# Optimization experiments

Hardware: AMD Instinct MI355X
Metric: run time of the kernel (lower is better)

Reference implementation:

```python
import jax, jax.numpy as jnp
import numpy as np
import math

B, S, D, H, DFF = 2, 2048, 1024, 16, 4096
DK = D // H
EPS = 1e-6


def setup_inputs() -> dict:
    key = jax.random.key(0)
    ks = jax.random.split(key, 12)
    s = 0.02
    return {
        "x": jax.random.normal(ks[0], (B, S, D), jnp.float32),
        "mask": jnp.ones((B, S), jnp.int32),
        "wq": jax.random.normal(ks[1], (D, D), jnp.float32) * s,
        "bq": jnp.zeros((D,), jnp.float32),
        "wk": jax.random.normal(ks[2], (D, D), jnp.float32) * s,
        "bk": jnp.zeros((D,), jnp.float32),
        "wv": jax.random.normal(ks[3], (D, D), jnp.float32) * s,
        "bv": jnp.zeros((D,), jnp.float32),
        "wo": jax.random.normal(ks[4], (D, D), jnp.float32) * s,
        "bo": jnp.zeros((D,), jnp.float32),
        "g1": jnp.ones((D,), jnp.float32),
        "b1": jnp.zeros((D,), jnp.float32),
        "g2": jnp.ones((D,), jnp.float32),
        "b2": jnp.zeros((D,), jnp.float32),
        "w1": jax.random.normal(ks[5], (DFF, D), jnp.float32) * s,
        "bf1": jnp.zeros((DFF,), jnp.float32),
        "w2": jax.random.normal(ks[6], (D, DFF), jnp.float32) * s,
        "bf2": jnp.zeros((D,), jnp.float32),
    }


def _gelu(x):
    # x * 0.5 * (1 + erf(x / sqrt(2))) -- exact erf-based GELU as in source
    return x * 0.5 * (1.0 + jax.lax.erf(x * (1.0 / math.sqrt(2.0))))


def _layernorm(x, gamma, beta):
    # torch.std uses unbiased (ddof=1); eps is OUTSIDE the sqrt in the source
    mean = jnp.mean(x, axis=-1, keepdims=True)
    std = jnp.std(x, axis=-1, keepdims=True, ddof=1)
    return gamma * (x - mean) / (std + EPS) + beta


def _block(x, mask, wq, bq, wk, bk, wv, bv, wo, bo, g1, b1, g2, b2, w1, bf1, w2, bf2):
    # multi-head attention (dropout is identity in eval mode)
    q = (x @ wq.T + bq).reshape(B, S, H, DK).transpose(0, 2, 1, 3)  # bhsd
    k = (x @ wk.T + bk).reshape(B, S, H, DK).transpose(0, 2, 1, 3)
    v = (x @ wv.T + bv).reshape(B, S, H, DK).transpose(0, 2, 1, 3)
    scores = jnp.einsum("bhsd,bhtd->bhst", q, k) / math.sqrt(DK)
    scores = jnp.where(mask[:, None, None, :] == 0, -1e9, scores)
    attn = jax.nn.softmax(scores, axis=-1)
    cv = jnp.einsum("bhst,bhtd->bhsd", attn, v)
    cv = cv.transpose(0, 2, 1, 3).reshape(B, S, D)
    hd = cv @ wo.T + bo
    # residual + norm1
    hd = _layernorm(x + hd, g1, b1)
    # position-wise FFN with erf GELU
    ff = _gelu(hd @ w1.T + bf1) @ w2.T + bf2
    return _layernorm(hd + ff, g2, b2)


def reference(x, mask, wq, bq, wk, bk, wv, bv, wo, bo, g1, b1, g2, b2, w1, bf1, w2, bf2):
    return _block(x, mask, wq, bq, wk, bk, wv, bv, wo, bo, g1, b1, g2, b2, w1, bf1, w2, bf2)
```

## Files before the change

### kernel.cpp

```cpp
#include <hip/hip_runtime.h>
#include <hip/hip_bf16.h>

#define B_   2
#define S_   2048
#define D_   1024
#define H_   16
#define DK_  64
#define DFF_ 4096
#define M_   (B_*S_)

typedef unsigned short u16;
typedef __attribute__((ext_vector_type(8))) short short8;
typedef __attribute__((ext_vector_type(4))) short bf16x4;
typedef __attribute__((ext_vector_type(4))) float floatx4;

__device__ __forceinline__ u16 f2bf(float f) {
    union { float f; unsigned u; } v; v.f = f;
    unsigned r = v.u + 0x7fffu + ((v.u >> 16) & 1u);
    return (u16)(r >> 16);
}
__device__ __forceinline__ u16 f2bf_fast(float f) {
    __hip_bfloat16 h = __float2bfloat16(f);
    return *reinterpret_cast<u16*>(&h);
}

__device__ __forceinline__ float exp2_fast(float f) {
    return __builtin_amdgcn_exp2f(f);
}

__device__ __forceinline__ void g2l16(const u16* g, u16* l) {
    __builtin_amdgcn_global_load_lds((const __attribute__((address_space(1))) void*)g,
                                     (__attribute__((address_space(3))) void*)l,
                                     16, 0, 0);
}

__device__ __forceinline__ unsigned lds_off(const void* p) {
    return (unsigned)(unsigned long long)p;
}

#define TRB16(dst, va, IMM)                                                    \
    asm volatile("ds_read_b64_tr_b16 %0, %1 offset:" #IMM                      \
                 : "=v"(dst) : "v"(va))

__global__ __launch_bounds__(256) void cvt_all(
    const float* __restrict__ x,  const float* __restrict__ wq,
    const float* __restrict__ wk, const float* __restrict__ wv,
    const float* __restrict__ wo, const float* __restrict__ w1,
    const float* __restrict__ w2,
    u16* __restrict__ xb, u16* __restrict__ wqkvb, u16* __restrict__ wob,
    u16* __restrict__ w1b, u16* __restrict__ w2b) {
    for (int i = blockIdx.x * 256 + threadIdx.x; i < 4194304;
         i += gridDim.x * 256) {
        const float* s; u16* d; int off;
        if (i < 1048576)      { s = x;  d = xb;    off = i; }
        else if (i < 1310720) { s = wq; d = wqkvb; off = i - 1048576; }
        else if (i < 1572864) { s = wk; d = wqkvb + 1048576; off = i - 1310720; }
        else if (i < 1835008) { s = wv; d = wqkvb + 2097152; off = i - 1572864; }
        else if (i < 2097152) { s = wo; d = wob;   off = i - 1835008; }
        else if (i < 3145728) { s = w1; d = w1b;   off = i - 2097152; }
        else                  { s = w2; d = w2b;   off = i - 3145728; }
        float4 v = reinterpret_cast<const float4*>(s)[off];
        ushort4 o;
        o.x = f2bf(v.x); o.y = f2bf(v.y); o.z = f2bf(v.z); o.w = f2bf(v.w);
        reinterpret_cast<ushort4*>(d)[off] = o;
    }
}

__global__ __launch_bounds__(256) void prep_misc(const float* __restrict__ bq,
                                                 const float* __restrict__ bk,
                                                 const float* __restrict__ bv,
                                                 const int* __restrict__ mask,
                                                 float* __restrict__ bqkv,
                                                 float* __restrict__ mbias) {
    int i = blockIdx.x * 256 + threadIdx.x;
    if (i < 3 * D_) {
        float v = (i < D_) ? bq[i] : (i < 2 * D_) ? bk[i - D_] : bv[i - 2 * D_];
        bqkv[i] = v;
    } else if (i < 3 * D_ + B_ * S_) {
        int k = i - 3 * D_;
        mbias[k] = (mask[k] == 0) ? -1.44269504e9f : 0.0f;
    }
}

template <int EPI>
__global__ __launch_bounds__(512, 2) void gemm256_bt(const u16* __restrict__ A,
                                                     const u16* __restrict__ Bw,
                                                     const float* __restrict__ bias,
                                                     u16* __restrict__ Cb,
                                                     int N, int K) {
    __shared__ alignas(16) u16 sA[2][2][8192];
    __shared__ alignas(16) u16 sB[2][2][8192];
    const int tid = threadIdx.x;
    const int wid = tid >> 6, lane = tid & 63;
    const int lrow = lane & 15, lgrp = lane >> 4;
    const int wm = wid >> 2, wn = wid & 3;

    const int nbx = gridDim.x;
    const int nwg = nbx * gridDim.y;
    const int orig = blockIdx.y * nbx + blockIdx.x;
    const int qd = nwg >> 3, rr = nwg & 7, xc = orig & 7, oi = orig >> 3;
    const int swz = (xc < rr ? xc * (qd + 1) : rr * (qd + 1) + (xc - rr) * qd) + oi;
    const int m0 = (swz % nbx) * 256, n0 = (swz / nbx) * 256;

    const u16* Ab = A + (size_t)m0 * K;
    const u16* Bb = Bw + (size_t)n0 * K;
    const int T = K >> 6;

    const int c0 = (wid * 2 + 0) * 64 + lane;
    const int c1 = (wid * 2 + 1) * 64 + lane;
    const int r0 = c0 >> 3, g0 = c0 & 7;
    const int r1 = c1 >> 3, g1 = c1 & 7;
    const size_t so0 = (size_t)r0 * K + (size_t)((g0 ^ (r0 & 7)) * 8);
    const size_t so1 = (size_t)r1 * K + (size_t)((g1 ^ (r1 & 7)) * 8);
    const int d0 = (wid * 2 + 0) * 512;
    const int d1 = (wid * 2 + 1) * 512;

    auto stageA = [&](int par, int half, int kt) {
        const u16* src = Ab + (size_t)(half * 128) * K + kt * 64;
        g2l16(src + so0, &sA[par][half][d0]);
        g2l16(src + so1, &sA[par][half][d1]);
    };
    auto stageB = [&](int par, int half, int kt) {
        const u16* src = Bb + (size_t)(half * 128) * K + kt * 64;
        g2l16(src + so0, &sB[par][half][d0]);
        g2l16(src + so1, &sB[par][half][d1]);
    };

    stageA(0, 0, 0); stageA(0, 1, 0);
    stageB(0, 0, 0); stageB(0, 1, 0);
    if (T > 1) { stageB(1, 0, 1); stageB(1, 1, 1); }
    asm volatile("s_waitcnt vmcnt(4)" ::: "memory");
    asm volatile("s_barrier" ::: "memory");

    floatx4 acc[8][4] = {};
    const int rbase = (wn & 1) * 64;
    const int bhalf = wn >> 1;

    for (int t = 0; t < T; t++) {
        const int par = t & 1;
        const char* baseA = (const char*)&sA[par][wm][0];
        const char* baseB = (const char*)&sB[par][bhalf][0];
        short8 bfr[4][2];
#pragma unroll
        for (int ph = 0; ph < 4; ph++) {
            if (ph == 0) {
#pragma unroll
                for (int nj = 0; nj < 4; nj++) {
                    int rb = rbase + nj * 16 + lrow;
#pragma unroll
                    for (int kk = 0; kk < 2; kk++) {
                        int off = rb * 128 + (((kk * 4 + lgrp) ^ (lrow & 7)) * 16);
                        bfr[nj][kk] = *reinterpret_cast<const short8*>(baseB + off);
                    }
                }
            }
            short8 af[2][2];
#pragma unroll
            for (int a = 0; a < 2; a++) {
                int ra = (2 * ph + a) * 16 + lrow;
#pragma unroll
                for (int kk = 0; kk < 2; kk++) {
                    int off = ra * 128 + (((kk * 4 + lgrp) ^ (lrow & 7)) * 16);
                    af[a][kk] = *reinterpret_cast<const short8*>(baseA + off);
                }
            }
            if (ph == 0) { if (t + 1 < T) stageA(par ^ 1, 0, t + 1); }
            if (ph == 1) { if (t + 1 < T) stageA(par ^ 1, 1, t + 1); }
            if (ph == 2) { if (t + 2 < T) stageB(par, 0, t + 2); }
            if (ph == 3) { if (t + 2 < T) stageB(par, 1, t + 2); }

            asm volatile("s_barrier" ::: "memory");
            asm volatile("s_waitcnt lgkmcnt(0)" ::: "memory");
            __builtin_amdgcn_sched_barrier(0);

            __builtin_amdgcn_s_setprio(1);
#pragma unroll
            for (int a = 0; a < 2; a++)
#pragma unroll
                for (int nj = 0; nj < 4; nj++) {
                    acc[2 * ph + a][nj] = __builtin_amdgcn_mfma_f32_16x16x32_bf16(
                        af[a][0], bfr[nj][0], acc[2 * ph + a][nj], 0, 0, 0);
                    acc[2 * ph + a][nj] = __builtin_amdgcn_mfma_f32_16x16x32_bf16(
                        af[a][1], bfr[nj][1], acc[2 * ph + a][nj], 0, 0, 0);
                }
            __builtin_amdgcn_s_setprio(0);

            if (ph == 3) {
                if (t >= T - 3) asm volatile("s_waitcnt vmcnt(0)" ::: "memory");
                else            asm volatile("s_waitcnt vmcnt(4)" ::: "memory");
            }
            asm volatile("s_barrier" ::: "memory");
        }
    }

#pragma unroll
    for (int mi = 0; mi < 8; mi++) {
        int row = m0 + wm * 128 + mi * 16 + lgrp * 4;
#pragma unroll
        for (int nj = 0; nj < 4; nj++) {
            int col = n0 + wn * 64 + nj * 16 + lrow;
            float bc = bias[col];
#pragma unroll
            for (int j = 0; j < 4; j++) {
                float v = acc[mi][nj][j] + bc;
                if (EPI == 2) v = 0.5f * v * (1.0f + erff(v * 0.70710678118654752f));
                Cb[(size_t)(row + j) * N + col] = f2bf(v);
            }
        }
    }
}

template <int SPLIT>
__global__ __launch_bounds__(256) void gemm_sk(const u16* __restrict__ A,
                                               const u16* __restrict__ Bw,
                                               const float* __restrict__ bias,
                                               float* __restrict__ Cf,
                                               int N, int K) {
    __shared__ u16 sA[128 * 32];
    __shared__ u16 sB[128 * 32];
    const int tid = threadIdx.x;
    const int wid = tid >> 6, lane = tid & 63;
    const int lrow = lane & 15, lgrp = lane >> 4;
    const int z = blockIdx.z;
    const int Kc = K / SPLIT;

    const int nbx = gridDim.x;
    const int nwg = nbx * gridDim.y;
    const int orig = blockIdx.y * nbx + blockIdx.x;
    const int qd = nwg >> 3, rr = nwg & 7, xc = orig & 7, oi = orig >> 3;
    const int swz = (xc < rr ? xc * (qd + 1) : rr * (qd + 1) + (xc - rr) * qd) + oi;
    const int m0 = (swz % nbx) * 128, n0 = (swz / nbx) * 128;

    const int wm = wid >> 1, wn = wid & 1;
    const int ar = lane >> 2, ac = lane & 3;

    floatx4 acc[4][4] = {};
    const u16* Ab = A + (size_t)m0 * K;
    const u16* Bb = Bw + (size_t)n0 * K;
    float* Co = Cf + (size_t)z * M_ * N;

    for (int k0 = z * Kc; k0 < (z + 1) * Kc; k0 += 32) {
#pragma unroll
        for (int i = 0; i < 2; i++) {
            int seg = wid * 2 + i;
            int row = seg * 16 + ar;
            g2l16(Ab + (size_t)row * K + k0 + ac * 8, &sA[seg * 512]);
            g2l16(Bb + (size_t)row * K + k0 + ac * 8, &sB[seg * 512]);
        }
        __syncthreads();
        short8 af[4], bfr[4];
#pragma unroll
        for (int mi = 0; mi < 4; mi++)
            af[mi] = *reinterpret_cast<const short8*>(
                &sA[(wm * 64 + mi * 16 + lrow) * 32 + lgrp * 8]);
#pragma unroll
        for (int ni = 0; ni < 4; ni++)
            bfr[ni] = *reinterpret_cast<const short8*>(
                &sB[(wn * 64 + ni * 16 + lrow) * 32 + lgrp * 8]);
#pragma unroll
        for (int mi = 0; mi < 4; mi++)
#pragma unroll
            for (int ni = 0; ni < 4; ni++)
                acc[mi][ni] = __builtin_amdgcn_mfma_f32_16x16x32_bf16(
                    af[mi], bfr[ni], acc[mi][ni], 0, 0, 0);
        __syncthreads();
    }

#pragma unroll
    for (int mi = 0; mi < 4; mi++) {
        int row = m0 + wm * 64 + mi * 16 + lgrp * 4;
#pragma unroll
        for (int ni = 0; ni < 4; ni++) {
            int col = n0 + wn * 64 + ni * 16 + lrow;
            float bc = (z == 0) ? bias[col] : 0.0f;
#pragma unroll
            for (int j = 0; j < 4; j++)
                Co[(size_t)(row + j) * N + col] = acc[mi][ni][j] + bc;
        }
    }
}

__global__ __launch_bounds__(512) void attn_kernel(const u16* __restrict__ QKV,
                                                   const float* __restrict__ mbias,
                                                   u16* __restrict__ O) {
    const int SD = 3 * D_;
    __shared__ alignas(16) u16 ktL[2][4096];
    __shared__ alignas(16) u16 vtL[2][4096];
    __shared__ alignas(16) u16 pL[8][1024];

    const int orig = blockIdx.y * gridDim.x + blockIdx.x;
    const int swz = (orig & 7) * 64 + (orig >> 3);
    const int qt = swz & 15, bh = swz >> 4;
    const int b = bh >> 4, h = bh & 15;

    const int tid = threadIdx.x, wid = tid >> 6, lane = tid & 63;
    const int lrow = lane & 15, lgrp = lane >> 4;

    const u16* Qp = QKV + h * DK_;
    const u16* Kp = QKV + D_ + h * DK_;
    const u16* Vp = QKV + 2 * D_ + h * DK_;
    const float* mbrow = mbias + b * S_;

    const int qr = qt * 128 + wid * 16 + lrow;
    const u16* qrow = Qp + (size_t)(b * S_ + qr) * SD;
    short8 aq0 = *reinterpret_cast<const short8*>(qrow + lgrp * 8);
    short8 aq1 = *reinterpret_cast<const short8*>(qrow + 32 + lgrp * 8);

    const int q8 = wid * 64 + lane;
    const int krow = q8 >> 3, kcb = q8 & 7;
    const u16* kq = Kp + (size_t)(b * S_ + krow) * SD + ((kcb ^ (krow & 7)) * 8);
    const int ov = wid * 512 + lane * 8;
    const int vk = ((ov >> 6) & 7) * 8 + ((ov >> 9) & 1) * 4 + ((ov >> 4) & 3);
    const int vd = (ov >> 10) * 16 + (ov & 8);
    const u16* vq = Vp + (size_t)(b * S_ + vk) * SD + vd;

    auto issue = [&](int bufIdx) {
        g2l16(kq, &ktL[bufIdx][wid * 512]);
        g2l16(vq, &vtL[bufIdx][wid * 512]);
        kq += 64 * SD;
        vq += 64 * SD;
    };

    floatx4 accO[4] = {};
    float mrun = -1e30f, lrun = 0.f;
    const float SC2 = 0.18033688011112042f;

    issue(0);
    int cur = 0;
    for (int t = 0; t < S_ / 64; t++) {
        const int kv0 = t * 64;
        if (t < S_ / 64 - 1) {
            issue(cur ^ 1);
            asm volatile("s_waitcnt vmcnt(2)" ::: "memory");
        } else {
            asm volatile("s_waitcnt vmcnt(0)" ::: "memory");
        }
        __builtin_amdgcn_s_barrier();
        asm volatile("" ::: "memory");

        const u16* ktc = ktL[cur];
        const unsigned vva = lds_off(vtL[cur]) + lane * 8;

        float4 mb[4];
#pragma unroll
        for (int ni = 0; ni < 4; ni++)
            mb[ni] = *reinterpret_cast<const float4*>(mbrow + kv0 + ni * 16 + lgrp * 4);

        floatx4 st[4];
        __builtin_amdgcn_s_setprio(1);
#pragma unroll
        for (int ni = 0; ni < 4; ni++) {
            int row = ni * 16 + lrow;
            int off0 = (row * 128 + lgrp * 16) ^ ((lrow & 7) << 4);
            int off1 = (row * 128 + 64 + lgrp * 16) ^ ((lrow & 7) << 4);
            short8 bk0 = *reinterpret_cast<const short8*>((const char*)ktc + off0);
            short8 bk1 = *reinterpret_cast<const short8*>((const char*)ktc + off1);
            floatx4 z = {0.f, 0.f, 0.f, 0.f};
            z = __builtin_amdgcn_mfma_f32_16x16x32_bf16(bk0, aq0, z, 0, 0, 0);
            z = __builtin_amdgcn_mfma_f32_16x16x32_bf16(bk1, aq1, z, 0, 0, 0);
            st[ni] = z;
        }
        __builtin_amdgcn_s_setprio(0);

        bf16x4 vt0[4], vt1[4], vt2[4], vt3[4];
#pragma unroll
        for (int nd = 0; nd < 4; nd++) {
            unsigned a = vva + nd * 2048;
            TRB16(vt0[nd], a, 0);
            TRB16(vt1[nd], a, 1024);
            TRB16(vt2[nd], a, 512);
            TRB16(vt3[nd], a, 1536);
        }

        float pm[4][4];
#pragma unroll
        for (int ni = 0; ni < 4; ni++) {
            const float* mbp = reinterpret_cast<const float*>(&mb[ni]);
#pragma unroll
            for (int j = 0; j < 4; j++)
                pm[ni][j] = fmaf(st[ni][j], SC2, mbp[j]);
        }
        float pmax = pm[0][0];
#pragma unroll
        for (int ni = 0; ni < 4; ni++)
#pragma unroll
            for (int j = 0; j < 4; j++) pmax = fmaxf(pmax, pm[ni][j]);
        pmax = fmaxf(pmax, __shfl_xor(pmax, 16, 64));
        pmax = fmaxf(pmax, __shfl_xor(pmax, 32, 64));

        bool upd = !__all(pmax - mrun <= 11.5f);
        float fac = 1.0f;
        if (upd) {
            float mn = fmaxf(mrun, pmax);
            fac = exp2_fast(mrun - mn);
            mrun = mn;
        }

        float p[4][4];
        float s = 0.f;
#pragma unroll
        for (int ni = 0; ni < 4; ni++)
#pragma unroll
            for (int j = 0; j < 4; j++) {
                float e = exp2_fast(pm[ni][j] - mrun);
                p[ni][j] = e;
                s += e;
            }
        s += __shfl_xor(s, 16, 64);
        s += __shfl_xor(s, 32, 64);
        lrun = lrun * fac + s;

#pragma unroll
        for (int ni = 0; ni < 4; ni++) {
            bf16x4 pw;
#pragma unroll
            for (int j = 0; j < 4; j++) pw[j] = (short)f2bf_fast(p[ni][j]);
            unsigned woff = (unsigned)((lrow * 128 + ni * 32 + lgrp * 8) ^ ((lrow & 7) << 4));
            *reinterpret_cast<bf16x4*>((char*)pL[wid] + woff) = pw;
        }

        if (upd) {
            float f0 = __shfl(fac, lgrp * 4 + 0, 64);
            float f1 = __shfl(fac, lgrp * 4 + 1, 64);
            float f2 = __shfl(fac, lgrp * 4 + 2, 64);
            float f3 = __shfl(fac, lgrp * 4 + 3, 64);
#pragma unroll
            for (int nd = 0; nd < 4; nd++) {
                floatx4 tt = accO[nd];
                tt[0] *= f0; tt[1] *= f1; tt[2] *= f2; tt[3] *= f3;
                accO[nd] = tt;
            }
        }

        asm volatile("s_waitcnt lgkmcnt(0)" ::: "memory");
        __builtin_amdgcn_sched_barrier(0);

        unsigned ra0 = (unsigned)((lrow * 128 + lgrp * 16) ^ ((lrow & 7) << 4));
        unsigned ra1 = (unsigned)((lrow * 128 + 64 + lgrp * 16) ^ ((lrow & 7) << 4));
        short8 ap0 = *reinterpret_cast<const short8*>((const char*)pL[wid] + ra0);
        short8 ap1 = *reinterpret_cast<const short8*>((const char*)pL[wid] + ra1);

        __builtin_amdgcn_s_setprio(1);
#pragma unroll
        for (int nd = 0; nd < 4; nd++) {
            short8 bv0 = __builtin_shufflevector(vt0[nd], vt1[nd], 0, 1, 2, 3, 4, 5, 6, 7);
            short8 bv1 = __builtin_shufflevector(vt2[nd], vt3[nd], 0, 1, 2, 3, 4, 5, 6, 7);
            accO[nd] = __builtin_amdgcn_mfma_f32_16x16x32_bf16(ap0, bv0, accO[nd], 0, 0, 0);
            accO[nd] = __builtin_amdgcn_mfma_f32_16x16x32_bf16(ap1, bv1, accO[nd], 0, 0, 0);
        }
        __builtin_amdgcn_s_setprio(0);

        asm volatile("" ::: "memory");
        __builtin_amdgcn_s_barrier();
        cur ^= 1;
    }

    float linv = 1.0f / lrun;
    float li[4];
#pragma unroll
    for (int j = 0; j < 4; j++) li[j] = __shfl(linv, lgrp * 4 + j, 64);
#pragma unroll
    for (int nd = 0; nd < 4; nd++)
#pragma unroll
        for (int j = 0; j < 4; j++) {
            int r = lgrp * 4 + j;
            float v = accO[nd][j] * li[j];
            O[(size_t)(b * S_ + qt * 128 + wid * 16 + r) * D_ + h * DK_ + nd * 16 + lrow] =
                f2bf_fast(v);
        }
}

template <int NR>
__global__ __launch_bounds__(256) void ln_kernel(const float* __restrict__ X,
                                                 const float* __restrict__ R0,
                                                 const float* __restrict__ R1,
                                                 const float* __restrict__ R2,
                                                 const float* __restrict__ R3,
                                                 const float* __restrict__ gam,
                                                 const float* __restrict__ bet,
                                                 float* __restrict__ outf,
                                                 u16* __restrict__ outb) {
    __shared__ float ws1[4], ws2[4];
    const int row = blockIdx.x, tid = threadIdx.x;
    const size_t ro = (size_t)row * D_;
    float4 v = reinterpret_cast<const float4*>(X + ro)[tid];
    {
        const float4 r = reinterpret_cast<const float4*>(R0 + ro)[tid];
        v.x += r.x; v.y += r.y; v.z += r.z; v.w += r.w;
    }
    if (NR >= 2) {
        const float4 r = reinterpret_cast<const float4*>(R1 + ro)[tid];
        v.x += r.x; v.y += r.y; v.z += r.z; v.w += r.w;
    }
    if (NR >= 3) {
        const float4 r = reinterpret_cast<const float4*>(R2 + ro)[tid];
        v.x += r.x; v.y += r.y; v.z += r.z; v.w += r.w;
    }
    if (NR >= 4) {
        const float4 r = reinterpret_cast<const float4*>(R3 + ro)[tid];
        v.x += r.x; v.y += r.y; v.z += r.z; v.w += r.w;
    }

    float s = v.x + v.y + v.z + v.w;
#pragma unroll
    for (int m = 32; m >= 1; m >>= 1) s += __shfl_xor(s, m, 64);
    if ((tid & 63) == 0) ws1[tid >> 6] = s;
    __syncthreads();
    float mean = (ws1[0] + ws1[1] + ws1[2] + ws1[3]) * (1.f / D_);

    float4 d; d.x = v.x - mean; d.y = v.y - mean; d.z = v.z - mean; d.w = v.w - mean;
    float q = d.x * d.x + d.y * d.y + d.z * d.z + d.w * d.w;
#pragma unroll
    for (int m = 32; m >= 1; m >>= 1) q += __shfl_xor(q, m, 64);
    if ((tid & 63) == 0) ws2[tid >> 6] = q;
    __syncthreads();
    float var = (ws2[0] + ws2[1] + ws2[2] + ws2[3]) * (1.f / (D_ - 1));
    float inv = 1.f / (sqrtf(var) + 1e-6f);

    const float4 g = reinterpret_cast<const float4*>(gam)[tid];
    const float4 bb = reinterpret_cast<const float4*>(bet)[tid];
    float4 o;
    o.x = g.x * d.x * inv + bb.x;
    o.y = g.y * d.y * inv + bb.y;
    o.z = g.z * d.z * inv + bb.z;
    o.w = g.w * d.w * inv + bb.w;
    if (outf) reinterpret_cast<float4*>(outf + ro)[tid] = o;
    if (outb) {
        ushort4 ob;
        ob.x = f2bf(o.x); ob.y = f2bf(o.y); ob.z = f2bf(o.z); ob.w = f2bf(o.w);
        reinterpret_cast<ushort4*>(outb + ro)[tid] = ob;
    }
}

extern "C" void kernel_launch(void* const* d_in, const int* in_sizes, int n_in,
                              void* d_out, int out_size, void* d_ws, size_t ws_size,
                              hipStream_t stream) {
    const float* x    = (const float*)d_in[0];
    const int*   mask = (const int*)d_in[1];
    const float* wq   = (const float*)d_in[2];
    const float* bq   = (const float*)d_in[3];
    const float* wk   = (const float*)d_in[4];
    const float* bk   = (const float*)d_in[5];
    const float* wv   = (const float*)d_in[6];
    const float* bv   = (const float*)d_in[7];
    const float* wo   = (const float*)d_in[8];
    const float* bo   = (const float*)d_in[9];
    const float* g1   = (const float*)d_in[10];
    const float* b1   = (const float*)d_in[11];
    const float* g2   = (const float*)d_in[12];
    const float* b2   = (const float*)d_in[13];
    const float* w1   = (const float*)d_in[14];
    const float* bf1  = (const float*)d_in[15];
    const float* w2   = (const float*)d_in[16];
    const float* bf2  = (const float*)d_in[17];
    float* out = (float*)d_out;

    char* ws = (char*)d_ws;
    const size_t MB = 1u << 20;
    u16*   xb    = (u16*)  (ws + 0 * MB);
    u16*   wqkvb = (u16*)  (ws + 8 * MB);
    u16*   qkvb  = (u16*)  (ws + 14 * MB);
    u16*   cvb   = (u16*)  (ws + 38 * MB);
    float* p0    = (float*)(ws + 46 * MB);
    float* p1    = (float*)(ws + 62 * MB);
    float* qpart = (float*)(ws + 0 * MB);
    u16*   wob   = (u16*)  (ws + 78 * MB);
    u16*   w1b   = (u16*)  (ws + 80 * MB);
    u16*   w2b   = (u16*)  (ws + 88 * MB);
    float* bqkv  = (float*)(ws + 96 * MB);
    float* mbias = (float*)(ws + 96 * MB + 65536);
    float* hdf   = (float*)(ws + 97 * MB);
    u16*   hdb   = (u16*)  (ws + 113 * MB);
    u16*   ff1b  = (u16*)  (ws + 121 * MB);

    cvt_all<<<2048, 256, 0, stream>>>(x, wq, wk, wv, wo, w1, w2,
                                      xb, wqkvb, wob, w1b, w2b);
    prep_misc<<<28, 256, 0, stream>>>(bq, bk, bv, mask, bqkv, mbias);

    gemm256_bt<0><<<dim3(M_ / 256, 3 * D_ / 256), 512, 0, stream>>>(
        xb, wqkvb, bqkv, qkvb, 3 * D_, D_);

    attn_kernel<<<dim3(S_ / 128, B_ * H_), 512, 0, stream>>>(qkvb, mbias, cvb);

    gemm_sk<2><<<dim3(M_ / 128, D_ / 128, 2), 256, 0, stream>>>(
        cvb, wob, bo, p0, D_, D_);

    ln_kernel<2><<<M_, 256, 0, stream>>>(x, p0, p1, nullptr, nullptr,
                                         g1, b1, hdf, hdb);

    gemm256_bt<2><<<dim3(M_ / 256, DFF_ / 256), 512, 0, stream>>>(
        hdb, w1b, bf1, ff1b, DFF_, D_);

    gemm_sk<4><<<dim3(M_ / 128, D_ / 128, 4), 256, 0, stream>>>(
        ff1b, w2b, bf2, qpart, D_, DFF_);

    ln_kernel<4><<<M_, 256, 0, stream>>>(hdf, qpart, qpart + (size_t)M_ * D_,
                                         qpart + 2 * (size_t)M_ * D_,
                                         qpart + 3 * (size_t)M_ * D_,
                                         g2, b2, out, nullptr);
}
```

Before: 410.6 us.

## Replace simple split-K GEMMs with pipelined 256-tile GEMM using split-K

```diff
diff --git a/kernel.cpp b/kernel.cpp
--- a/kernel.cpp
+++ b/kernel.cpp
@@ -23,17 +23,14 @@
     __hip_bfloat16 h = __float2bfloat16(f);
     return *reinterpret_cast<u16*>(&h);
 }
-
 __device__ __forceinline__ float exp2_fast(float f) {
     return __builtin_amdgcn_exp2f(f);
 }
-
 __device__ __forceinline__ void g2l16(const u16* g, u16* l) {
     __builtin_amdgcn_global_load_lds((const __attribute__((address_space(1))) void*)g,
                                      (__attribute__((address_space(3))) void*)l,
                                      16, 0, 0);
 }
-
 __device__ __forceinline__ unsigned lds_off(const void* p) {
     return (unsigned)(unsigned long long)p;
 }
@@ -87,6 +84,7 @@
                                                      const u16* __restrict__ Bw,
                                                      const float* __restrict__ bias,
                                                      u16* __restrict__ Cb,
+                                                     float* __restrict__ Cf,
                                                      int N, int K) {
     __shared__ alignas(16) u16 sA[2][2][8192];
     __shared__ alignas(16) u16 sB[2][2][8192];
@@ -94,17 +92,20 @@
     const int wid = tid >> 6, lane = tid & 63;
     const int lrow = lane & 15, lgrp = lane >> 4;
     const int wm = wid >> 2, wn = wid & 3;
-
-    const int nbx = gridDim.x;
-    const int nwg = nbx * gridDim.y;
+    const int z = blockIdx.z;
+    const int Kc = K / gridDim.z;
+    const int zbase = z * Kc;
+
+    const int nbx = gridDim.x, nby = gridDim.y;
+    const int nwg = nbx * nby;
     const int orig = blockIdx.y * nbx + blockIdx.x;
     const int qd = nwg >> 3, rr = nwg & 7, xc = orig & 7, oi = orig >> 3;
     const int swz = (xc < rr ? xc * (qd + 1) : rr * (qd + 1) + (xc - rr) * qd) + oi;
-    const int m0 = (swz % nbx) * 256, n0 = (swz / nbx) * 256;
-
-    const u16* Ab = A + (size_t)m0 * K;
-    const u16* Bb = Bw + (size_t)n0 * K;
-    const int T = K >> 6;
+    const int m0 = (swz / nby) * 256, n0 = (swz % nby) * 256;
+
+    const u16* Ab = A + (size_t)m0 * K + zbase;
+    const u16* Bb = Bw + (size_t)n0 * K + zbase;
+    const int T = Kc >> 6;
 
     const int c0 = (wid * 2 + 0) * 64 + lane;
     const int c1 = (wid * 2 + 1) * 64 + lane;
@@ -193,89 +194,23 @@
         }
     }
 
+    float* Co = (EPI == 1) ? Cf + (size_t)z * M_ * N : nullptr;
 #pragma unroll
     for (int mi = 0; mi < 8; mi++) {
         int row = m0 + wm * 128 + mi * 16 + lgrp * 4;
 #pragma unroll
         for (int nj = 0; nj < 4; nj++) {
             int col = n0 + wn * 64 + nj * 16 + lrow;
-            float bc = bias[col];
+            float bc = (EPI != 1 || z == 0) ? bias[col] : 0.0f;
 #pragma unroll
             for (int j = 0; j < 4; j++) {
                 float v = acc[mi][nj][j] + bc;
                 if (EPI == 2) v = 0.5f * v * (1.0f + erff(v * 0.70710678118654752f));
-                Cb[(size_t)(row + j) * N + col] = f2bf(v);
+                if (EPI == 1)
+                    Co[(size_t)(row + j) * N + col] = v;
+                else
+                    Cb[(size_t)(row + j) * N + col] = f2bf(v);
             }
-        }
-    }
-}
-
-template <int SPLIT>
-__global__ __launch_bounds__(256) void gemm_sk(const u16* __restrict__ A,
-                                               const u16* __restrict__ Bw,
-                                               const float* __restrict__ bias,
-                                               float* __restrict__ Cf,
-                                               int N, int K) {
-    __shared__ u16 sA[128 * 32];
-    __shared__ u16 sB[128 * 32];
-    const int tid = threadIdx.x;
-    const int wid = tid >> 6, lane = tid & 63;
-    const int lrow = lane & 15, lgrp = lane >> 4;
-    const int z = blockIdx.z;
-    const int Kc = K / SPLIT;
-
-    const int nbx = gridDim.x;
-    const int nwg = nbx * gridDim.y;
-    const int orig = blockIdx.y * nbx + blockIdx.x;
-    const int qd = nwg >> 3, rr = nwg & 7, xc = orig & 7, oi = orig >> 3;
-    const int swz = (xc < rr ? xc * (qd + 1) : rr * (qd + 1) + (xc - rr) * qd) + oi;
-    const int m0 = (swz % nbx) * 128, n0 = (swz / nbx) * 128;
-
-    const int wm = wid >> 1, wn = wid & 1;
-    const int ar = lane >> 2, ac = lane & 3;
-
-    floatx4 acc[4][4] = {};
-    const u16* Ab = A + (size_t)m0 * K;
-    const u16* Bb = Bw + (size_t)n0 * K;
-    float* Co = Cf + (size_t)z * M_ * N;
-
-    for (int k0 = z * Kc; k0 < (z + 1) * Kc; k0 += 32) {
-#pragma unroll
-        for (int i = 0; i < 2; i++) {
-            int seg = wid * 2 + i;
-            int row = seg * 16 + ar;
-            g2l16(Ab + (size_t)row * K + k0 + ac * 8, &sA[seg * 512]);
-            g2l16(Bb + (size_t)row * K + k0 + ac * 8, &sB[seg * 512]);
-        }
-        __syncthreads();
-        short8 af[4], bfr[4];
-#pragma unroll
-        for (int mi = 0; mi < 4; mi++)
-            af[mi] = *reinterpret_cast<const short8*>(
-                &sA[(wm * 64 + mi * 16 + lrow) * 32 + lgrp * 8]);
-#pragma unroll
-        for (int ni = 0; ni < 4; ni++)
-            bfr[ni] = *reinterpret_cast<const short8*>(
-                &sB[(wn * 64 + ni * 16 + lrow) * 32 + lgrp * 8]);
-#pragma unroll
-        for (int mi = 0; mi < 4; mi++)
-#pragma unroll
-            for (int ni = 0; ni < 4; ni++)
-                acc[mi][ni] = __builtin_amdgcn_mfma_f32_16x16x32_bf16(
-                    af[mi], bfr[ni], acc[mi][ni], 0, 0, 0);
-        __syncthreads();
-    }
-
-#pragma unroll
-    for (int mi = 0; mi < 4; mi++) {
-        int row = m0 + wm * 64 + mi * 16 + lgrp * 4;
-#pragma unroll
-        for (int ni = 0; ni < 4; ni++) {
-            int col = n0 + wn * 64 + ni * 16 + lrow;
-            float bc = (z == 0) ? bias[col] : 0.0f;
-#pragma unroll
-            for (int j = 0; j < 4; j++)
-                Co[(size_t)(row + j) * N + col] = acc[mi][ni][j] + bc;
         }
     }
 }
@@ -560,39 +495,40 @@
     u16*   xb    = (u16*)  (ws + 0 * MB);
     u16*   wqkvb = (u16*)  (ws + 8 * MB);
     u16*   qkvb  = (u16*)  (ws + 14 * MB);
-    u16*   cvb   = (u16*)  (ws + 38 * MB);
-    float* p0    = (float*)(ws + 46 * MB);
-    float* p1    = (float*)(ws + 62 * MB);
+    u16*   cvb   = (u16*)  (ws + 64 * MB);
+    float* pp    = (float*)(ws + 0 * MB);
     float* qpart = (float*)(ws + 0 * MB);
-    u16*   wob   = (u16*)  (ws + 78 * MB);
-    u16*   w1b   = (u16*)  (ws + 80 * MB);
-    u16*   w2b   = (u16*)  (ws + 88 * MB);
-    float* bqkv  = (float*)(ws + 96 * MB);
-    float* mbias = (float*)(ws + 96 * MB + 65536);
-    float* hdf   = (float*)(ws + 97 * MB);
-    u16*   hdb   = (u16*)  (ws + 113 * MB);
-    u16*   ff1b  = (u16*)  (ws + 121 * MB);
+    u16*   wob   = (u16*)  (ws + 72 * MB);
+    u16*   w1b   = (u16*)  (ws + 74 * MB);
+    u16*   w2b   = (u16*)  (ws + 82 * MB);
+    float* bqkv  = (float*)(ws + 90 * MB);
+    float* mbias = (float*)(ws + 90 * MB + 65536);
+    float* hdf   = (float*)(ws + 91 * MB);
+    u16*   hdb   = (u16*)  (ws + 107 * MB);
+    u16*   ff1b  = (u16*)  (ws + 115 * MB);
 
     cvt_all<<<2048, 256, 0, stream>>>(x, wq, wk, wv, wo, w1, w2,
                                       xb, wqkvb, wob, w1b, w2b);
     prep_misc<<<28, 256, 0, stream>>>(bq, bk, bv, mask, bqkv, mbias);
 
-    gemm256_bt<0><<<dim3(M_ / 256, 3 * D_ / 256), 512, 0, stream>>>(
-        xb, wqkvb, bqkv, qkvb, 3 * D_, D_);
+    gemm256_bt<0><<<dim3(M_ / 256, 3 * D_ / 256, 1), 512, 0, stream>>>(
+        xb, wqkvb, bqkv, qkvb, nullptr, 3 * D_, D_);
 
     attn_kernel<<<dim3(S_ / 128, B_ * H_), 512, 0, stream>>>(qkvb, mbias, cvb);
 
-    gemm_sk<2><<<dim3(M_ / 128, D_ / 128, 2), 256, 0, stream>>>(
-        cvb, wob, bo, p0, D_, D_);
-
-    ln_kernel<2><<<M_, 256, 0, stream>>>(x, p0, p1, nullptr, nullptr,
+    gemm256_bt<1><<<dim3(M_ / 256, D_ / 256, 4), 512, 0, stream>>>(
+        cvb, wob, bo, nullptr, pp, D_, D_);
+
+    ln_kernel<4><<<M_, 256, 0, stream>>>(x, pp, pp + (size_t)M_ * D_,
+                                         pp + 2 * (size_t)M_ * D_,
+                                         pp + 3 * (size_t)M_ * D_,
                                          g1, b1, hdf, hdb);
 
-    gemm256_bt<2><<<dim3(M_ / 256, DFF_ / 256), 512, 0, stream>>>(
-        hdb, w1b, bf1, ff1b, DFF_, D_);
-
-    gemm_sk<4><<<dim3(M_ / 128, D_ / 128, 4), 256, 0, stream>>>(
-        ff1b, w2b, bf2, qpart, D_, DFF_);
+    gemm256_bt<2><<<dim3(M_ / 256, DFF_ / 256, 1), 512, 0, stream>>>(
+        hdb, w1b, bf1, ff1b, nullptr, DFF_, D_);
+
+    gemm256_bt<1><<<dim3(M_ / 256, D_ / 256, 4), 512, 0, stream>>>(
+        ff1b, w2b, bf2, nullptr, qpart, D_, DFF_);
 
     ln_kernel<4><<<M_, 256, 0, stream>>>(hdf, qpart, qpart + (size_t)M_ * D_,
                                          qpart + 2 * (size_t)M_ * D_,
```

Result: faster. 381.6 us (-7.1%).
